# Kernel optimization log

Hardware: AMD Instinct MI355X
Metric: run time of the kernel (lower is better)

Reference implementation:

```python
import jax, jax.numpy as jnp
import numpy as np
import math

N_HEAD = 16  # from init_kwargs

def setup_inputs() -> dict:
    key = jax.random.key(0)
    ks = jax.random.split(key, 11)
    B, T, D = 2, 2048, 1024
    s = 0.02
    return {
        "q": jax.random.normal(ks[0], (B, T, D), jnp.float32),
        "k": jax.random.normal(ks[1], (B, T, D), jnp.float32),
        "v": jax.random.normal(ks[2], (B, T, D), jnp.float32),
        "Wq": jax.random.normal(ks[3], (D, D), jnp.float32) * s,
        "bq": jax.random.normal(ks[4], (D,), jnp.float32) * s,
        "Wk": jax.random.normal(ks[5], (D, D), jnp.float32) * s,
        "bk": jax.random.normal(ks[6], (D,), jnp.float32) * s,
        "Wv": jax.random.normal(ks[7], (D, D), jnp.float32) * s,
        "bv": jax.random.normal(ks[8], (D,), jnp.float32) * s,
        "Wc": jax.random.normal(ks[9], (D, D), jnp.float32) * s,
        "bc": jax.random.normal(ks[10], (D,), jnp.float32) * s,
    }

def reference(q, k, v, Wq, bq, Wk, bk, Wv, bv, Wc, bc):
    B, T, D = q.shape
    H = N_HEAD
    nd = D // H

    def proj(x, W, b):
        # torch Linear: x @ W.T + b; then split heads -> [b, h, t, nd]
        y = x @ W.T + b
        return y.reshape(B, T, H, nd).transpose(0, 2, 1, 3)

    qh = proj(q, Wq, bq)
    kh = proj(k, Wk, bk)
    vh = proj(v, Wv, bv)

    # scores: [b, h, t_q, t_k]
    z = jnp.einsum('bhqd,bhkd->bhqk', qh, kh) / math.sqrt(nd)
    mask = jnp.tril(jnp.ones((T, T), dtype=bool))  # causal
    z = jnp.where(mask, z, -jnp.inf)
    # NOTE: original uses nn.Softmax(dim=-2) -> softmax over the QUERY axis
    attn = jax.nn.softmax(z, axis=-2)
    out = jnp.einsum('bhqk,bhkd->bhqd', attn, vh)  # [b, h, t, nd]
    out = out.transpose(0, 2, 1, 3).reshape(B, T, D)
    return out @ Wc.T + bc
```

## Files before the change

kernel.cpp:

```cpp
#include <hip/hip_runtime.h>


#define Dd 1024
#define Tt 2048
#define Bb 2
#define Hh 16
#define NDh 64
#define Mm (Bb * Tt)

using u16 = unsigned short;
using u32 = unsigned int;
typedef __attribute__((ext_vector_type(8))) short bf16x8;
typedef __attribute__((ext_vector_type(4))) float f32x4;

__device__ __forceinline__ u16 f2bf(float f) {
  return (u16)((__float_as_uint(f) + 0x8000u) >> 16);
}
__device__ __forceinline__ float fexp2(float x) {
  return __builtin_amdgcn_exp2f(x);
}
__device__ __forceinline__ void ldsdma16(const u16* g, u16* l) {
  __builtin_amdgcn_global_load_lds(
      (const __attribute__((address_space(1))) u32*)g,
      (__attribute__((address_space(3))) u32*)l, 16, 0, 0);
}
#define MFMA(a, b, c) __builtin_amdgcn_mfma_f32_16x16x32_bf16((a), (b), (c), 0, 0, 0)
__device__ __forceinline__ bf16x8 ldfrag(const u16* lds, int row, int kgrp) {
  return *(const bf16x8*)(lds + row * 64 + (((kgrp) ^ (row & 7)) * 8));
}

__global__ __launch_bounds__(256) void cvt_all(
    const float* __restrict__ w0, const float* __restrict__ w1,
    const float* __restrict__ w2, const float* __restrict__ w3,
    const float* __restrict__ q, const float* __restrict__ k,
    const float* __restrict__ v,
    u16* __restrict__ Wb, u16* __restrict__ Xb,
    float* __restrict__ outz, float* __restrict__ lsumz)
{
  const int vid = blockIdx.x * 256 + threadIdx.x;
  const float* s;
  u16* d;
  if (vid < (1 << 20)) {
    const int seg = vid >> 18, off = (vid & 0x3FFFF) * 4;
    s = (seg == 0 ? w0 : seg == 1 ? w1 : seg == 2 ? w2 : w3) + off;
    d = Wb + (size_t)seg * Dd * Dd + off;
    *(float4*)(outz + (size_t)vid * 4) = make_float4(0.f, 0.f, 0.f, 0.f);
    if (vid < Bb * Hh * Tt / 4)
      *(float4*)(lsumz + (size_t)vid * 4) = make_float4(0.f, 0.f, 0.f, 0.f);
  } else {
    const int iv = vid - (1 << 20);
    const int seg = iv >> 20, off = (iv & 0xFFFFF) * 4;
    s = (seg == 0 ? q : seg == 1 ? k : v) + off;
    d = Xb + (size_t)seg * Mm * Dd + off;
  }
  float4 f = *(const float4*)s;
  ushort4 o;
  o.x = f2bf(f.x); o.y = f2bf(f.y); o.z = f2bf(f.z); o.w = f2bf(f.w);
  *(ushort4*)d = o;
}

__device__ __forceinline__ void gemm_body(
    const u16* __restrict__ X, const u16* __restrict__ WB,
    const float* __restrict__ bias, void* Yv, float oscale,
    int omode, int kc, int knum, u16* As, u16* Bs)
{
  const int t = threadIdx.x, lane = t & 63, w = t >> 6;
  const int col = lane & 15, quad = lane >> 4;
  const int m0 = blockIdx.x * 128, n0 = blockIdx.y * 128;
  const int wm = (w >> 1) * 64, wn = (w & 1) * 64;
  const int drr = lane >> 3, dsw = ((lane & 7) ^ drr) * 8;
  const int kbeg = (Dd / knum) * kc, kend = kbeg + Dd / knum;

  f32x4 acc[4][4] = {};

  for (int k0 = kbeg; k0 < kend; k0 += 64) {
    __syncthreads();
#pragma unroll
    for (int i = 0; i < 4; i++) {
      const int rr = w * 32 + i * 8;
      ldsdma16(X + (size_t)(m0 + rr + drr) * Dd + k0 + dsw, As + rr * 64);
      ldsdma16(WB + (size_t)(n0 + rr + drr) * Dd + k0 + dsw, Bs + rr * 64);
    }
    __syncthreads();
#pragma unroll
    for (int s = 0; s < 2; s++) {
      bf16x8 a[4], b[4];
#pragma unroll
      for (int i = 0; i < 4; i++)
        a[i] = ldfrag(As, wm + i * 16 + col, s * 4 + quad);
#pragma unroll
      for (int j = 0; j < 4; j++)
        b[j] = ldfrag(Bs, wn + j * 16 + col, s * 4 + quad);
#pragma unroll
      for (int i = 0; i < 4; i++)
#pragma unroll
        for (int j = 0; j < 4; j++)
          acc[i][j] = MFMA(a[i], b[j], acc[i][j]);
    }
  }

#pragma unroll
  for (int jt = 0; jt < 4; jt++) {
    const int n = n0 + wn + jt * 16 + col;
    const float bn = (omode == 2 && kc != 0) ? 0.f : bias[n];
    if (omode == 1) {
#pragma unroll
      for (int i = 0; i < 4; i++) {
        const int mg = m0 + wm + i * 16 + quad * 4;
        const int bb = mg >> 11, tl = mg & 2047;
        ushort4 o;
        o.x = f2bf(acc[i][jt][0] + bn);
        o.y = f2bf(acc[i][jt][1] + bn);
        o.z = f2bf(acc[i][jt][2] + bn);
        o.w = f2bf(acc[i][jt][3] + bn);
        *(ushort4*)((u16*)Yv + (size_t)bb * Dd * Tt + (size_t)n * Tt + tl) = o;
      }
    } else if (omode == 0) {
      u16* Y = (u16*)Yv;
#pragma unroll
      for (int i = 0; i < 4; i++)
#pragma unroll
        for (int r = 0; r < 4; r++) {
          const int m = m0 + wm + i * 16 + quad * 4 + r;
          Y[(size_t)m * Dd + n] = f2bf((acc[i][jt][r] + bn) * oscale);
        }
    } else {
      float* Y = (float*)Yv;
#pragma unroll
      for (int i = 0; i < 4; i++)
#pragma unroll
        for (int r = 0; r < 4; r++) {
          const int m = m0 + wm + i * 16 + quad * 4 + r;
          atomicAdd(&Y[(size_t)m * Dd + n], acc[i][jt][r] + bn);
        }
    }
  }
}

__global__ __launch_bounds__(256) void proj_qkv(
    const u16* __restrict__ Xb, const u16* __restrict__ Wb,
    const float* __restrict__ bq, const float* __restrict__ bk,
    const float* __restrict__ bv,
    u16* __restrict__ Qp, u16* __restrict__ Kp, u16* __restrict__ VtG)
{
  __shared__ u16 As[128 * 64];
  __shared__ u16 Bs[128 * 64];
  const int z = blockIdx.z;
  const u16* X = Xb + (size_t)z * Mm * Dd;
  const u16* W = Wb + (size_t)z * Dd * Dd;
  const float* bias = z == 0 ? bq : z == 1 ? bk : bv;
  void* Y = z == 0 ? (void*)Qp : z == 1 ? (void*)Kp : (void*)VtG;
  const float qs = 0.125f * 1.44269504088896f;
  gemm_body(X, W, bias, Y, z == 0 ? qs : 1.0f, z == 2 ? 1 : 0, 0, 1, As, Bs);
}

__global__ __launch_bounds__(256) void gemm_final(
    const u16* __restrict__ Ctx, const u16* __restrict__ Wcb,
    const float* __restrict__ bc, float* __restrict__ out)
{
  __shared__ u16 As[128 * 64];
  __shared__ u16 Bs[128 * 64];
  gemm_body(Ctx, Wcb, bc, out, 1.0f, 2, blockIdx.z, 2, As, Bs);
}

__global__ __launch_bounds__(256) void attn_stats(
    const u16* __restrict__ Qp, const u16* __restrict__ Kp,
    float* __restrict__ lsum)
{
  __shared__ u16 Ks[128 * 64];
  __shared__ u16 Qs[128 * 64];
  const int t = threadIdx.x, lane = t & 63, w = t >> 6;
  const int col = lane & 15, quad = lane >> 4;
  const int bh = blockIdx.x, b = bh >> 4, h = bh & 15;
  const int j = blockIdx.y, tk0 = j * 128, c = blockIdx.z;
  const u16* Kbase = Kp + (size_t)b * Tt * Dd + h * NDh;
  const u16* Qbase = Qp + (size_t)b * Tt * Dd + h * NDh;
  const int drr = lane >> 3, dsw = ((lane & 7) ^ drr) * 8;

#pragma unroll
  for (int i = 0; i < 4; i++) {
    const int rr = w * 32 + i * 8;
    ldsdma16(Kbase + (size_t)(tk0 + rr + drr) * Dd + dsw, Ks + rr * 64);
  }
  __syncthreads();
  bf16x8 ka[2][2];
#pragma unroll
  for (int s2 = 0; s2 < 2; s2++) {
    const int row = w * 32 + s2 * 16 + col;
    ka[s2][0] = ldfrag(Ks, row, quad);
    ka[s2][1] = ldfrag(Ks, row, 4 + quad);
  }

  float l[2][4] = {};

  for (int jj = j + c; jj < Tt / 128; jj += 2) {
    const bool masked = (jj == j);
    const int tq0 = jj * 128;
    __syncthreads();
#pragma unroll
    for (int i = 0; i < 4; i++) {
      const int rr = w * 32 + i * 8;
      ldsdma16(Qbase + (size_t)(tq0 + rr + drr) * Dd + dsw, Qs + rr * 64);
    }
    __syncthreads();
#pragma unroll
    for (int jt = 0; jt < 8; jt++) {
      bf16x8 qb0 = ldfrag(Qs, jt * 16 + col, quad);
      bf16x8 qb1 = ldfrag(Qs, jt * 16 + col, 4 + quad);
      const int tq = tq0 + jt * 16 + col;
#pragma unroll
      for (int s2 = 0; s2 < 2; s2++) {
        f32x4 z = {};
        z = MFMA(ka[s2][0], qb0, z);
        z = MFMA(ka[s2][1], qb1, z);
#pragma unroll
        for (int r = 0; r < 4; r++) {
          float e = fexp2(z[r]);
          if (masked) {
            const int tk = tk0 + w * 32 + s2 * 16 + quad * 4 + r;
            e = (tq >= tk) ? e : 0.f;
          }
          l[s2][r] += e;
        }
      }
    }
  }

#pragma unroll
  for (int s2 = 0; s2 < 2; s2++)
#pragma unroll
    for (int r = 0; r < 4; r++) {
      float s = l[s2][r];
#pragma unroll
      for (int m = 1; m < 16; m <<= 1) s += __shfl_xor(s, m);
      if (col == 0)
        atomicAdd(&lsum[(size_t)bh * Tt + tk0 + w * 32 + s2 * 16 + quad * 4 + r], s);
    }
}

__global__ __launch_bounds__(256) void attn_out(
    const u16* __restrict__ Qp, const u16* __restrict__ Kp,
    const u16* __restrict__ VtG, const float* __restrict__ lsum,
    u16* __restrict__ Ctx)
{
  __shared__ u16 QPs[128 * 64];
  __shared__ u16 Ks[64 * 64];
  __shared__ u16 Vts[64 * 64];
  __shared__ float srl[64];
  const int t = threadIdx.x, lane = t & 63, w = t >> 6;
  const int col = lane & 15, quad = lane >> 4;
  const int bh = blockIdx.x, b = bh >> 4, h = bh & 15;
  const int tq0 = (gridDim.y - 1 - blockIdx.y) * 128;
  const u16* Qbase = Qp + (size_t)b * Tt * Dd + h * NDh;
  const u16* Kbase = Kp + (size_t)b * Tt * Dd + h * NDh;
  const u16* Vbase = VtG + (size_t)b * Dd * Tt + (size_t)h * NDh * Tt;
  const int drr = lane >> 3, dsw = ((lane & 7) ^ drr) * 8;

#pragma unroll
  for (int i = 0; i < 4; i++) {
    const int rr = w * 32 + i * 8;
    ldsdma16(Qbase + (size_t)(tq0 + rr + drr) * Dd + dsw, QPs + rr * 64);
  }
  __syncthreads();
  bf16x8 qa[2][2];
#pragma unroll
  for (int s2 = 0; s2 < 2; s2++) {
    const int row = w * 32 + s2 * 16 + col;
    qa[s2][0] = ldfrag(QPs, row, quad);
    qa[s2][1] = ldfrag(QPs, row, 4 + quad);
  }

  f32x4 o[2][4] = {};

  for (int tk0 = 0; tk0 < tq0 + 128; tk0 += 64) {
    const bool masked = (tk0 >= tq0);
    __syncthreads();
#pragma unroll
    for (int i = 0; i < 2; i++) {
      const int rr = w * 16 + i * 8;
      ldsdma16(Kbase + (size_t)(tk0 + rr + drr) * Dd + dsw, Ks + rr * 64);
      ldsdma16(Vbase + (size_t)(rr + drr) * Tt + tk0 + dsw, Vts + rr * 64);
    }
    if (t < 64) srl[t] = 1.0f / lsum[(size_t)bh * Tt + tk0 + t];
    __syncthreads();
#pragma unroll
    for (int jt = 0; jt < 4; jt++) {
      bf16x8 kb0 = ldfrag(Ks, jt * 16 + col, quad);
      bf16x8 kb1 = ldfrag(Ks, jt * 16 + col, 4 + quad);
      const int tkl = jt * 16 + col;
      const float rl = srl[tkl];
#pragma unroll
      for (int s2 = 0; s2 < 2; s2++) {
        f32x4 z = {};
        z = MFMA(qa[s2][0], kb0, z);
        z = MFMA(qa[s2][1], kb1, z);
#pragma unroll
        for (int r = 0; r < 4; r++) {
          const int row = w * 32 + s2 * 16 + quad * 4 + r;
          float p = fexp2(z[r]) * rl;
          if (masked) p = (tk0 + tkl <= tq0 + row) ? p : 0.f;
          QPs[row * 64 + (((tkl >> 3) ^ (row & 7)) * 8) + (tkl & 7)] = f2bf(p);
        }
      }
    }
    bf16x8 pa[2][2];
#pragma unroll
    for (int s2 = 0; s2 < 2; s2++) {
      const int row = w * 32 + s2 * 16 + col;
      pa[s2][0] = ldfrag(QPs, row, quad);
      pa[s2][1] = ldfrag(QPs, row, 4 + quad);
    }
#pragma unroll
    for (int dn = 0; dn < 4; dn++) {
      bf16x8 vb0 = ldfrag(Vts, dn * 16 + col, quad);
      bf16x8 vb1 = ldfrag(Vts, dn * 16 + col, 4 + quad);
#pragma unroll
      for (int s2 = 0; s2 < 2; s2++) {
        o[s2][dn] = MFMA(pa[s2][0], vb0, o[s2][dn]);
        o[s2][dn] = MFMA(pa[s2][1], vb1, o[s2][dn]);
      }
    }
  }

#pragma unroll
  for (int s2 = 0; s2 < 2; s2++)
#pragma unroll
    for (int dn = 0; dn < 4; dn++)
#pragma unroll
      for (int r = 0; r < 4; r++) {
        const int tq = tq0 + w * 32 + s2 * 16 + quad * 4 + r;
        Ctx[(size_t)(b * Tt + tq) * Dd + h * NDh + dn * 16 + col] = f2bf(o[s2][dn][r]);
      }
}

extern "C" void kernel_launch(void* const* d_in, const int* in_sizes, int n_in,
                              void* d_out, int out_size, void* d_ws, size_t ws_size,
                              hipStream_t stream)
{
  const float* q  = (const float*)d_in[0];
  const float* k  = (const float*)d_in[1];
  const float* v  = (const float*)d_in[2];
  const float* Wq = (const float*)d_in[3];
  const float* bq = (const float*)d_in[4];
  const float* Wk = (const float*)d_in[5];
  const float* bk = (const float*)d_in[6];
  const float* Wv = (const float*)d_in[7];
  const float* bv = (const float*)d_in[8];
  const float* Wc = (const float*)d_in[9];
  const float* bc = (const float*)d_in[10];

  u16* Wb   = (u16*)d_ws;
  u16* Xb   = Wb + (size_t)4 * Dd * Dd;
  u16* Qp   = Xb + (size_t)3 * Mm * Dd;
  u16* Kp   = Qp + (size_t)Mm * Dd;
  u16* VtG  = Kp + (size_t)Mm * Dd;
  u16* Ctx  = VtG + (size_t)Mm * Dd;
  float* lsum = (float*)(Ctx + (size_t)Mm * Dd);

  cvt_all<<<16384, 256, 0, stream>>>(Wq, Wk, Wv, Wc, q, k, v, Wb, Xb,
                                     (float*)d_out, lsum);
  proj_qkv<<<dim3(Mm / 128, Dd / 128, 3), 256, 0, stream>>>(
      Xb, Wb, bq, bk, bv, Qp, Kp, VtG);
  attn_stats<<<dim3(Bb * Hh, Tt / 128, 2), 256, 0, stream>>>(Qp, Kp, lsum);
  attn_out<<<dim3(Bb * Hh, Tt / 128), 256, 0, stream>>>(Qp, Kp, VtG, lsum, Ctx);
  gemm_final<<<dim3(Mm / 128, Dd / 128, 2), 256, 0, stream>>>(
      Ctx, Wb + (size_t)3 * Dd * Dd, bc, (float*)d_out);
}
```

Before: 276.3 us.

## Split attention output over key halves with fp32 atomic accumulation

The attn_out kernel now splits each query tile's key loop across two blocks that interleave key chunks. It accumulates partial outputs into an fp32 buffer with atomicAdd. The buffer is zeroed inside attn_stats and reuses the Xb workspace, and a new kernel converts it to bf16 before the final GEMM. The goal is more blocks and better balance for the causal workload. In exchange it adds atomic traffic, an extra conversion launch and extra memory passes.

```diff
diff --git a/kernel.cpp b/kernel.cpp
--- a/kernel.cpp
+++ b/kernel.cpp
@@ -163,9 +163,19 @@
   gemm_body(Ctx, Wcb, bc, out, 1.0f, 2, blockIdx.z, 2, As, Bs);
 }
 
+__global__ __launch_bounds__(256) void cvt_ctx(
+    const float* __restrict__ Ctx32, u16* __restrict__ Ctxb)
+{
+  const int vid = blockIdx.x * 256 + threadIdx.x;
+  float4 f = *(const float4*)(Ctx32 + (size_t)vid * 4);
+  ushort4 o;
+  o.x = f2bf(f.x); o.y = f2bf(f.y); o.z = f2bf(f.z); o.w = f2bf(f.w);
+  *(ushort4*)(Ctxb + (size_t)vid * 4) = o;
+}
+
 __global__ __launch_bounds__(256) void attn_stats(
     const u16* __restrict__ Qp, const u16* __restrict__ Kp,
-    float* __restrict__ lsum)
+    float* __restrict__ lsum, float* __restrict__ Ctx32z)
 {
   __shared__ u16 Ks[128 * 64];
   __shared__ u16 Qs[128 * 64];
@@ -177,6 +187,15 @@
   const u16* Qbase = Qp + (size_t)b * Tt * Dd + h * NDh;
   const int drr = lane >> 3, dsw = ((lane & 7) ^ drr) * 8;
 
+  {
+    const size_t zid = ((size_t)(blockIdx.z * gridDim.y + blockIdx.y) * gridDim.x
+                        + blockIdx.x) * 256 + t;
+#pragma unroll
+    for (int i = 0; i < 4; i++)
+      *(float4*)(Ctx32z + (zid + (size_t)i * 262144) * 4) =
+          make_float4(0.f, 0.f, 0.f, 0.f);
+  }
+
 #pragma unroll
   for (int i = 0; i < 4; i++) {
     const int rr = w * 32 + i * 8;
@@ -241,7 +260,7 @@
 __global__ __launch_bounds__(256) void attn_out(
     const u16* __restrict__ Qp, const u16* __restrict__ Kp,
     const u16* __restrict__ VtG, const float* __restrict__ lsum,
-    u16* __restrict__ Ctx)
+    float* __restrict__ Ctx32)
 {
   __shared__ u16 QPs[128 * 64];
   __shared__ u16 Ks[64 * 64];
@@ -251,6 +270,7 @@
   const int col = lane & 15, quad = lane >> 4;
   const int bh = blockIdx.x, b = bh >> 4, h = bh & 15;
   const int tq0 = (gridDim.y - 1 - blockIdx.y) * 128;
+  const int c = blockIdx.z;
   const u16* Qbase = Qp + (size_t)b * Tt * Dd + h * NDh;
   const u16* Kbase = Kp + (size_t)b * Tt * Dd + h * NDh;
   const u16* Vbase = VtG + (size_t)b * Dd * Tt + (size_t)h * NDh * Tt;
@@ -272,7 +292,8 @@
 
   f32x4 o[2][4] = {};
 
-  for (int tk0 = 0; tk0 < tq0 + 128; tk0 += 64) {
+  for (int it = c; it * 64 < tq0 + 128; it += 2) {
+    const int tk0 = it * 64;
     const bool masked = (tk0 >= tq0);
     __syncthreads();
 #pragma unroll
@@ -329,7 +350,8 @@
 #pragma unroll
       for (int r = 0; r < 4; r++) {
         const int tq = tq0 + w * 32 + s2 * 16 + quad * 4 + r;
-        Ctx[(size_t)(b * Tt + tq) * Dd + h * NDh + dn * 16 + col] = f2bf(o[s2][dn][r]);
+        atomicAdd(&Ctx32[(size_t)(b * Tt + tq) * Dd + h * NDh + dn * 16 + col],
+                  o[s2][dn][r]);
       }
 }
 
@@ -351,18 +373,20 @@
 
   u16* Wb   = (u16*)d_ws;
   u16* Xb   = Wb + (size_t)4 * Dd * Dd;
+  float* Ctx32 = (float*)Xb;
   u16* Qp   = Xb + (size_t)3 * Mm * Dd;
   u16* Kp   = Qp + (size_t)Mm * Dd;
   u16* VtG  = Kp + (size_t)Mm * Dd;
-  u16* Ctx  = VtG + (size_t)Mm * Dd;
-  float* lsum = (float*)(Ctx + (size_t)Mm * Dd);
+  u16* Ctxb = VtG + (size_t)Mm * Dd;
+  float* lsum = (float*)(Ctxb + (size_t)Mm * Dd);
 
   cvt_all<<<16384, 256, 0, stream>>>(Wq, Wk, Wv, Wc, q, k, v, Wb, Xb,
                                      (float*)d_out, lsum);
   proj_qkv<<<dim3(Mm / 128, Dd / 128, 3), 256, 0, stream>>>(
       Xb, Wb, bq, bk, bv, Qp, Kp, VtG);
-  attn_stats<<<dim3(Bb * Hh, Tt / 128, 2), 256, 0, stream>>>(Qp, Kp, lsum);
-  attn_out<<<dim3(Bb * Hh, Tt / 128), 256, 0, stream>>>(Qp, Kp, VtG, lsum, Ctx);
+  attn_stats<<<dim3(Bb * Hh, Tt / 128, 2), 256, 0, stream>>>(Qp, Kp, lsum, Ctx32);
+  attn_out<<<dim3(Bb * Hh, Tt / 128, 2), 256, 0, stream>>>(Qp, Kp, VtG, lsum, Ctx32);
+  cvt_ctx<<<4096, 256, 0, stream>>>(Ctx32, Ctxb);
   gemm_final<<<dim3(Mm / 128, Dd / 128, 2), 256, 0, stream>>>(
-      Ctx, Wb + (size_t)3 * Dd * Dd, bc, (float*)d_out);
-}
+      Ctxb, Wb + (size_t)3 * Dd * Dd, bc, (float*)d_out);
+}
```

Measured after the change: 270.5 us. -2.1%, faster.

## Split attention KV loop across two blocks and fold 1/lsum into V

Applied to the files above, without the earlier changes.

The attention output kernel now splits the key loop across two blocks, which write fp32 partial contexts. The last-arriving block of each pair, detected with an atomic counter, sums the partials into a bf16 context. The per-key normalization 1/lsum is applied once to V^T by the last attn_stats block per key tile, which removes the per-iteration reciprocal load from the inner loop. The final GEMM's split-K factor also goes from 2 to 4. These changes aim to double attention parallelism and improve load balance, at the cost of extra fp32 traffic, atomics and a workspace that reuses the Xb region.

```diff
diff --git a/kernel.cpp b/kernel.cpp
--- a/kernel.cpp
+++ b/kernel.cpp
@@ -19,6 +19,8 @@
 __device__ __forceinline__ float fexp2(float x) {
   return __builtin_amdgcn_exp2f(x);
 }
+__device__ __forceinline__ float bfl(u32 u) { return __uint_as_float(u << 16); }
+__device__ __forceinline__ float bfh(u32 u) { return __uint_as_float(u & 0xffff0000u); }
 __device__ __forceinline__ void ldsdma16(const u16* g, u16* l) {
   __builtin_amdgcn_global_load_lds(
       (const __attribute__((address_space(1))) u32*)g,
@@ -35,7 +37,7 @@
     const float* __restrict__ q, const float* __restrict__ k,
     const float* __restrict__ v,
     u16* __restrict__ Wb, u16* __restrict__ Xb,
-    float* __restrict__ outz, float* __restrict__ lsumz)
+    float* __restrict__ outz, float* __restrict__ lsumz, int* __restrict__ cnt)
 {
   const int vid = blockIdx.x * 256 + threadIdx.x;
   const float* s;
@@ -47,6 +49,7 @@
     *(float4*)(outz + (size_t)vid * 4) = make_float4(0.f, 0.f, 0.f, 0.f);
     if (vid < Bb * Hh * Tt / 4)
       *(float4*)(lsumz + (size_t)vid * 4) = make_float4(0.f, 0.f, 0.f, 0.f);
+    if (vid < 256) *(int4*)(cnt + vid * 4) = make_int4(0, 0, 0, 0);
   } else {
     const int iv = vid - (1 << 20);
     const int seg = iv >> 20, off = (iv & 0xFFFFF) * 4;
@@ -160,15 +163,16 @@
 {
   __shared__ u16 As[128 * 64];
   __shared__ u16 Bs[128 * 64];
-  gemm_body(Ctx, Wcb, bc, out, 1.0f, 2, blockIdx.z, 2, As, Bs);
+  gemm_body(Ctx, Wcb, bc, out, 1.0f, 2, blockIdx.z, 4, As, Bs);
 }
 
 __global__ __launch_bounds__(256) void attn_stats(
     const u16* __restrict__ Qp, const u16* __restrict__ Kp,
-    float* __restrict__ lsum)
+    float* __restrict__ lsum, u16* __restrict__ VtG, int* __restrict__ cnt1)
 {
   __shared__ u16 Ks[128 * 64];
   __shared__ u16 Qs[128 * 64];
+  __shared__ int rank;
   const int t = threadIdx.x, lane = t & 63, w = t >> 6;
   const int col = lane & 15, quad = lane >> 4;
   const int bh = blockIdx.x, b = bh >> 4, h = bh & 15;
@@ -236,21 +240,53 @@
       if (col == 0)
         atomicAdd(&lsum[(size_t)bh * Tt + tk0 + w * 32 + s2 * 16 + quad * 4 + r], s);
     }
+
+  __syncthreads();
+  if (t == 0) {
+    __threadfence();
+    rank = atomicAdd(&cnt1[bh * 16 + j], 1);
+  }
+  __syncthreads();
+  if (rank == 1) {
+    __threadfence();
+    const int d = t >> 2, cb = (t & 3) * 32;
+    u16* vp = VtG + ((size_t)b * Dd + h * NDh + d) * Tt + tk0 + cb;
+    const float* lp = lsum + (size_t)bh * Tt + tk0 + cb;
+#pragma unroll
+    for (int u = 0; u < 4; u++) {
+      uint4 vv = *(uint4*)(vp + u * 8);
+      float4 l0 = *(const float4*)(lp + u * 8);
+      float4 l1 = *(const float4*)(lp + u * 8 + 4);
+      uint4 o;
+      o.x = (u32)f2bf(bfl(vv.x) * __builtin_amdgcn_rcpf(l0.x)) |
+            ((u32)f2bf(bfh(vv.x) * __builtin_amdgcn_rcpf(l0.y)) << 16);
+      o.y = (u32)f2bf(bfl(vv.y) * __builtin_amdgcn_rcpf(l0.z)) |
+            ((u32)f2bf(bfh(vv.y) * __builtin_amdgcn_rcpf(l0.w)) << 16);
+      o.z = (u32)f2bf(bfl(vv.z) * __builtin_amdgcn_rcpf(l1.x)) |
+            ((u32)f2bf(bfh(vv.z) * __builtin_amdgcn_rcpf(l1.y)) << 16);
+      o.w = (u32)f2bf(bfl(vv.w) * __builtin_amdgcn_rcpf(l1.z)) |
+            ((u32)f2bf(bfh(vv.w) * __builtin_amdgcn_rcpf(l1.w)) << 16);
+      *(uint4*)(vp + u * 8) = o;
+    }
+  }
 }
 
 __global__ __launch_bounds__(256) void attn_out(
     const u16* __restrict__ Qp, const u16* __restrict__ Kp,
-    const u16* __restrict__ VtG, const float* __restrict__ lsum,
-    u16* __restrict__ Ctx)
+    const u16* __restrict__ VtG,
+    float* __restrict__ Ca, float* __restrict__ Cb,
+    u16* __restrict__ Ctxb, int* __restrict__ cnt2)
 {
   __shared__ u16 QPs[128 * 64];
   __shared__ u16 Ks[64 * 64];
   __shared__ u16 Vts[64 * 64];
-  __shared__ float srl[64];
+  __shared__ int rank;
   const int t = threadIdx.x, lane = t & 63, w = t >> 6;
   const int col = lane & 15, quad = lane >> 4;
   const int bh = blockIdx.x, b = bh >> 4, h = bh & 15;
   const int tq0 = (gridDim.y - 1 - blockIdx.y) * 128;
+  const int c = blockIdx.z;
+  float* dst = c == 0 ? Ca : Cb;
   const u16* Qbase = Qp + (size_t)b * Tt * Dd + h * NDh;
   const u16* Kbase = Kp + (size_t)b * Tt * Dd + h * NDh;
   const u16* Vbase = VtG + (size_t)b * Dd * Tt + (size_t)h * NDh * Tt;
@@ -272,7 +308,8 @@
 
   f32x4 o[2][4] = {};
 
-  for (int tk0 = 0; tk0 < tq0 + 128; tk0 += 64) {
+  for (int it = c; it * 64 < tq0 + 128; it += 2) {
+    const int tk0 = it * 64;
     const bool masked = (tk0 >= tq0);
     __syncthreads();
 #pragma unroll
@@ -281,14 +318,12 @@
       ldsdma16(Kbase + (size_t)(tk0 + rr + drr) * Dd + dsw, Ks + rr * 64);
       ldsdma16(Vbase + (size_t)(rr + drr) * Tt + tk0 + dsw, Vts + rr * 64);
     }
-    if (t < 64) srl[t] = 1.0f / lsum[(size_t)bh * Tt + tk0 + t];
     __syncthreads();
 #pragma unroll
     for (int jt = 0; jt < 4; jt++) {
       bf16x8 kb0 = ldfrag(Ks, jt * 16 + col, quad);
       bf16x8 kb1 = ldfrag(Ks, jt * 16 + col, 4 + quad);
       const int tkl = jt * 16 + col;
-      const float rl = srl[tkl];
 #pragma unroll
       for (int s2 = 0; s2 < 2; s2++) {
         f32x4 z = {};
@@ -297,7 +332,7 @@
 #pragma unroll
         for (int r = 0; r < 4; r++) {
           const int row = w * 32 + s2 * 16 + quad * 4 + r;
-          float p = fexp2(z[r]) * rl;
+          float p = fexp2(z[r]);
           if (masked) p = (tk0 + tkl <= tq0 + row) ? p : 0.f;
           QPs[row * 64 + (((tkl >> 3) ^ (row & 7)) * 8) + (tkl & 7)] = f2bf(p);
         }
@@ -329,8 +364,29 @@
 #pragma unroll
       for (int r = 0; r < 4; r++) {
         const int tq = tq0 + w * 32 + s2 * 16 + quad * 4 + r;
-        Ctx[(size_t)(b * Tt + tq) * Dd + h * NDh + dn * 16 + col] = f2bf(o[s2][dn][r]);
+        dst[(size_t)(b * Tt + tq) * Dd + h * NDh + dn * 16 + col] = o[s2][dn][r];
       }
+
+  __syncthreads();
+  if (t == 0) {
+    __threadfence();
+    rank = atomicAdd(&cnt2[bh * 16 + blockIdx.y], 1);
+  }
+  __syncthreads();
+  if (rank == 1) {
+    __threadfence();
+    const int rr = t >> 1, cb2 = (t & 1) * 32;
+    const size_t base = (size_t)(b * Tt + tq0 + rr) * Dd + h * NDh + cb2;
+#pragma unroll
+    for (int u = 0; u < 8; u++) {
+      float4 a = *(const float4*)(Ca + base + u * 4);
+      float4 bx = *(const float4*)(Cb + base + u * 4);
+      ushort4 oo;
+      oo.x = f2bf(a.x + bx.x); oo.y = f2bf(a.y + bx.y);
+      oo.z = f2bf(a.z + bx.z); oo.w = f2bf(a.w + bx.w);
+      *(ushort4*)(Ctxb + base + u * 4) = oo;
+    }
+  }
 }
 
 extern "C" void kernel_launch(void* const* d_in, const int* in_sizes, int n_in,
@@ -351,18 +407,25 @@
 
   u16* Wb   = (u16*)d_ws;
   u16* Xb   = Wb + (size_t)4 * Dd * Dd;
+  float* Ctx32a = (float*)Xb;
   u16* Qp   = Xb + (size_t)3 * Mm * Dd;
   u16* Kp   = Qp + (size_t)Mm * Dd;
   u16* VtG  = Kp + (size_t)Mm * Dd;
-  u16* Ctx  = VtG + (size_t)Mm * Dd;
-  float* lsum = (float*)(Ctx + (size_t)Mm * Dd);
+  u16* Ctxb = VtG + (size_t)Mm * Dd;
+  float* lsum = (float*)(Ctxb + (size_t)Mm * Dd);
+  float* Ctx32b = lsum + (size_t)Bb * Hh * Tt;
+  int* cnt = (int*)(Ctx32b + (size_t)Mm * Dd);
+  int* cnt1 = cnt;
+  int* cnt2 = cnt + 512;
 
   cvt_all<<<16384, 256, 0, stream>>>(Wq, Wk, Wv, Wc, q, k, v, Wb, Xb,
-                                     (float*)d_out, lsum);
+                                     (float*)d_out, lsum, cnt);
   proj_qkv<<<dim3(Mm / 128, Dd / 128, 3), 256, 0, stream>>>(
       Xb, Wb, bq, bk, bv, Qp, Kp, VtG);
-  attn_stats<<<dim3(Bb * Hh, Tt / 128, 2), 256, 0, stream>>>(Qp, Kp, lsum);
-  attn_out<<<dim3(Bb * Hh, Tt / 128), 256, 0, stream>>>(Qp, Kp, VtG, lsum, Ctx);
-  gemm_final<<<dim3(Mm / 128, Dd / 128, 2), 256, 0, stream>>>(
-      Ctx, Wb + (size_t)3 * Dd * Dd, bc, (float*)d_out);
-}
+  attn_stats<<<dim3(Bb * Hh, Tt / 128, 2), 256, 0, stream>>>(
+      Qp, Kp, lsum, VtG, cnt1);
+  attn_out<<<dim3(Bb * Hh, Tt / 128, 2), 256, 0, stream>>>(
+      Qp, Kp, VtG, Ctx32a, Ctx32b, Ctxb, cnt2);
+  gemm_final<<<dim3(Mm / 128, Dd / 128, 4), 256, 0, stream>>>(
+      Ctxb, Wb + (size_t)3 * Dd * Dd, bc, (float*)d_out);
+}
```

Measured after the change: 482.7 us. 1.75x slower.
